# Kernel tuning notes

Measured on AMD Instinct MI355X. Metric: run time of the kernel, lower is better.

## Reference

```python
import jax, jax.numpy as jnp
import numpy as np

K_HOPS = 3  # spektral TAGConv default
BN_EPS = 1e-3  # keras BatchNormalization default epsilon


def _propagate(x, edge_src, edge_dst, edge_weight, n_nodes):
    # y[dst] += w * x[src]  (sparse adjacency @ x)
    msg = x[edge_src] * edge_weight[:, None]
    return jax.ops.segment_sum(msg, edge_dst, num_segments=n_nodes)


def _tag_conv(x, edge_src, edge_dst, edge_weight, W, b):
    n = x.shape[0]
    hops = [x]
    h = x
    for _ in range(K_HOPS):
        h = _propagate(h, edge_src, edge_dst, edge_weight, n)
        hops.append(h)
    # concat hops along features then dense combine: [N, F*(K+1)] @ [F*(K+1), C]
    return jnp.concatenate(hops, axis=-1) @ W + b


def setup_inputs() -> dict:
    key = jax.random.key(0)
    ks = jax.random.split(key, 6)
    N, F, E, H, L = 20000, 2000, 640000, 128, 15
    x = jax.random.normal(ks[0], (N, F), dtype=jnp.float32)
    edge_src = jax.random.randint(ks[1], (E,), 0, N, dtype=jnp.int32)
    edge_dst = jax.random.randint(ks[2], (E,), 0, N, dtype=jnp.int32)
    # normalized adjacency weights, roughly 1/avg_degree scale
    edge_weight = jax.random.uniform(ks[3], (E,), dtype=jnp.float32) / 32.0
    W1 = jax.random.normal(ks[4], (F * (K_HOPS + 1), H), dtype=jnp.float32) * (1.0 / np.sqrt(F * (K_HOPS + 1)))
    b1 = jnp.zeros((H,), dtype=jnp.float32)
    gamma = jnp.ones((H,), dtype=jnp.float32)
    beta = jnp.zeros((H,), dtype=jnp.float32)
    moving_mean = jnp.zeros((H,), dtype=jnp.float32)
    moving_var = jnp.ones((H,), dtype=jnp.float32)
    W2 = jax.random.normal(ks[5], (H * (K_HOPS + 1), L), dtype=jnp.float32) * (1.0 / np.sqrt(H * (K_HOPS + 1)))
    b2 = jnp.zeros((L,), dtype=jnp.float32)
    return {"x": x, "edge_src": edge_src, "edge_dst": edge_dst, "edge_weight": edge_weight,
            "W1": W1, "b1": b1, "gamma": gamma, "beta": beta,
            "moving_mean": moving_mean, "moving_var": moving_var, "W2": W2, "b2": b2}


def reference(x, edge_src, edge_dst, edge_weight, W1, b1, gamma, beta,
              moving_mean, moving_var, W2, b2):
    # training=False: Dropout is identity, BN uses moving statistics
    h = _tag_conv(x, edge_src, edge_dst, edge_weight, W1, b1)
    h = (h - moving_mean) * jax.lax.rsqrt(moving_var + BN_EPS) * gamma + beta
    h = jax.nn.relu(h)
    z = _tag_conv(h, edge_src, edge_dst, edge_weight, W2, b2)
    return z
```

## Files before the change

kernel.cpp:

```cpp
#include <hip/hip_runtime.h>
#include <cstdint>
#include <cstddef>

#define N_NODES 20000
#define F_IN    2000
#define H_DIM   128
#define L_DIM   15
#define K_PAD   2048
#define M_PAD   20096
#define N1      512
#define BM      128
#define BN      128
#define BK      32

typedef __attribute__((ext_vector_type(4))) float f32x4;
typedef __attribute__((ext_vector_type(8))) short s16x8;
typedef __attribute__((ext_vector_type(8))) unsigned short u16x8;

__device__ __forceinline__ unsigned short f2bf(float f) {
  unsigned int u = __float_as_uint(f);
  u += 0x7fff + ((u >> 16) & 1);
  return (unsigned short)(u >> 16);
}

__global__ __launch_bounds__(256) void k_cvt_x(const float* __restrict__ x,
                                               unsigned short* __restrict__ xb) {
  unsigned int t = blockIdx.x * 256u + threadIdx.x;
  unsigned int row = t >> 8;
  unsigned int colB = (t & 255u) * 8u;
  u16x8 o = {0, 0, 0, 0, 0, 0, 0, 0};
  if (row < N_NODES && colB < F_IN) {
    const float4 a = *(const float4*)(x + (size_t)row * F_IN + colB);
    const float4 b = *(const float4*)(x + (size_t)row * F_IN + colB + 4);
    o[0] = f2bf(a.x); o[1] = f2bf(a.y); o[2] = f2bf(a.z); o[3] = f2bf(a.w);
    o[4] = f2bf(b.x); o[5] = f2bf(b.y); o[6] = f2bf(b.z); o[7] = f2bf(b.w);
  }
  *(u16x8*)(xb + (size_t)t * 8) = o;
}

__global__ __launch_bounds__(256) void k_cvt_w1(const float* __restrict__ W1,
                                                unsigned short* __restrict__ bt) {
  __shared__ unsigned short tile[128 * 67];
  const int hop = blockIdx.x >> 5;
  const int k0  = (blockIdx.x & 31) * 64;
  const int t = threadIdx.x;
#pragma unroll
  for (int it = 0; it < 8; ++it) {
    int f4 = it * 256 + t;
    int r  = f4 >> 5;
    int c4 = f4 & 31;
    int k = k0 + r;
    float4 v = make_float4(0.f, 0.f, 0.f, 0.f);
    if (k < F_IN) v = *(const float4*)(W1 + (size_t)(hop * F_IN + k) * H_DIM + c4 * 4);
    tile[(c4 * 4 + 0) * 67 + r] = f2bf(v.x);
    tile[(c4 * 4 + 1) * 67 + r] = f2bf(v.y);
    tile[(c4 * 4 + 2) * 67 + r] = f2bf(v.z);
    tile[(c4 * 4 + 3) * 67 + r] = f2bf(v.w);
  }
  __syncthreads();
  const int c = t >> 1, kh = (t & 1) * 32;
  unsigned short* dst = bt + (size_t)(hop * 128 + c) * K_PAD + k0 + kh;
  const unsigned short* srcp = tile + c * 67 + kh;
#pragma unroll
  for (int q = 0; q < 4; ++q) {
    u16x8 o;
#pragma unroll
    for (int e = 0; e < 8; ++e) o[e] = srcp[q * 8 + e];
    *(u16x8*)(dst + q * 8) = o;
  }
}

__global__ __launch_bounds__(256) void k_gemm1(const unsigned short* __restrict__ A,
                                               const unsigned short* __restrict__ B,
                                               float* __restrict__ C) {
  __shared__ unsigned short As[BM * BK];
  __shared__ unsigned short Bs[BN * BK];
  const int b = blockIdx.x;
  const int i_tile = (b & 7) + 8 * (b >> 5);
  const int j_tile = (b >> 3) & 3;
  if (i_tile >= M_PAD / BM) return;
  const int rowA0 = i_tile * BM;
  const int colB0 = j_tile * BN;
  const int tid  = threadIdx.x;
  const int lane = tid & 63;
  const int wave = tid >> 6;
  const int wm = (wave >> 1) * 64;
  const int wn = (wave & 1) * 64;
  const int quad = lane >> 4;
  const int l15  = lane & 15;
  f32x4 acc[4][4] = {};

  for (int kt = 0; kt < K_PAD; kt += BK) {
#pragma unroll
    for (int r = 0; r < 2; ++r) {
      int c = r * 256 + tid;
      int row = c >> 2;
      int kc = (c & 3) * 8;
      const unsigned short* ga = A + (size_t)(rowA0 + row) * K_PAD + kt + kc;
      __builtin_amdgcn_global_load_lds((const __attribute__((address_space(1))) void*)ga,
                                       (__attribute__((address_space(3))) void*)(As + c * 8),
                                       16, 0, 0);
      const unsigned short* gb = B + (size_t)(colB0 + row) * K_PAD + kt + kc;
      __builtin_amdgcn_global_load_lds((const __attribute__((address_space(1))) void*)gb,
                                       (__attribute__((address_space(3))) void*)(Bs + c * 8),
                                       16, 0, 0);
    }
    __syncthreads();
    s16x8 af[4], bfr[4];
#pragma unroll
    for (int i = 0; i < 4; ++i)
      af[i] = *(const s16x8*)(As + (wm + i * 16 + l15) * BK + quad * 8);
#pragma unroll
    for (int j = 0; j < 4; ++j)
      bfr[j] = *(const s16x8*)(Bs + (wn + j * 16 + l15) * BK + quad * 8);
#pragma unroll
    for (int i = 0; i < 4; ++i)
#pragma unroll
      for (int j = 0; j < 4; ++j)
        acc[i][j] = __builtin_amdgcn_mfma_f32_16x16x32_bf16(af[i], bfr[j], acc[i][j], 0, 0, 0);
    __syncthreads();
  }

#pragma unroll
  for (int i = 0; i < 4; ++i) {
    int row0 = rowA0 + wm + i * 16 + quad * 4;
#pragma unroll
    for (int j = 0; j < 4; ++j) {
      int col = colB0 + wn + j * 16 + l15;
#pragma unroll
      for (int r = 0; r < 4; ++r) {
        int row = row0 + r;
        if (row < N_NODES) C[(size_t)row * N1 + col] = acc[i][j][r];
      }
    }
  }
}

__global__ __launch_bounds__(256) void k_hist(const int* __restrict__ dst,
                                              int* __restrict__ deg, int E) {
  int i = blockIdx.x * 256 + threadIdx.x;
  int e = i * 4;
  if (e + 4 <= E) {
    int4 d4 = *(const int4*)(dst + e);
    atomicAdd(&deg[d4.x], 1); atomicAdd(&deg[d4.y], 1);
    atomicAdd(&deg[d4.z], 1); atomicAdd(&deg[d4.w], 1);
  } else {
    for (; e < E; ++e) atomicAdd(&deg[dst[e]], 1);
  }
}

__global__ __launch_bounds__(1024) void k_scan(const int* __restrict__ deg,
                                               int* __restrict__ rowStart,
                                               int* __restrict__ cursor) {
  __shared__ int sums[1024];
  const int t = threadIdx.x;
  const int chunk = (N_NODES + 1023) / 1024;
  int lo = t * chunk;
  int hi = lo + chunk; if (hi > N_NODES) hi = N_NODES;
  int s = 0;
  for (int i = lo; i < hi; ++i) s += deg[i];
  sums[t] = s;
  __syncthreads();
  for (int off = 1; off < 1024; off <<= 1) {
    int v = sums[t];
    int u = (t >= off) ? sums[t - off] : 0;
    __syncthreads();
    sums[t] = v + u;
    __syncthreads();
  }
  int run = sums[t] - s;
  for (int i = lo; i < hi; ++i) {
    rowStart[i] = run; cursor[i] = run; run += deg[i];
  }
  if (t == 1023) rowStart[N_NODES] = run;
}

__global__ __launch_bounds__(256) void k_scatter(const int* __restrict__ src,
                                                 const int* __restrict__ dst,
                                                 const float* __restrict__ w,
                                                 int* cursor,
                                                 int2* __restrict__ eSW, int E) {
  int e = blockIdx.x * 256 + threadIdx.x;
  if (e >= E) return;
  int p = atomicAdd(&cursor[dst[e]], 1);
  eSW[p] = make_int2(src[e], __float_as_int(w[e]));
}

__global__ __launch_bounds__(256) void k_prop128(const int* __restrict__ rowStart,
    const int2* __restrict__ eSW,
    const float* __restrict__ in, int inStride, int inOff,
    const float* __restrict__ addv, int addStride, int addOff,
    float* __restrict__ out,
    const float* __restrict__ b1, const float* __restrict__ gamma,
    const float* __restrict__ beta, const float* __restrict__ mean,
    const float* __restrict__ var, int doBN) {
  const int lane = threadIdx.x & 63;
  const int d = blockIdx.x * 4 + (threadIdx.x >> 6);
  const int s0 = rowStart[d], s1 = rowStart[d + 1];
  const int c2 = lane * 2;
  float2 acc = make_float2(0.f, 0.f);
  int j = s0;
  for (; j + 8 <= s1; j += 8) {
    int2 e0 = eSW[j],     e1 = eSW[j + 1], e2 = eSW[j + 2], e3 = eSW[j + 3];
    int2 e4 = eSW[j + 4], e5 = eSW[j + 5], e6 = eSW[j + 6], e7 = eSW[j + 7];
    float2 v0 = *(const float2*)(in + (size_t)e0.x * inStride + inOff + c2);
    float2 v1 = *(const float2*)(in + (size_t)e1.x * inStride + inOff + c2);
    float2 v2 = *(const float2*)(in + (size_t)e2.x * inStride + inOff + c2);
    float2 v3 = *(const float2*)(in + (size_t)e3.x * inStride + inOff + c2);
    float2 v4 = *(const float2*)(in + (size_t)e4.x * inStride + inOff + c2);
    float2 v5 = *(const float2*)(in + (size_t)e5.x * inStride + inOff + c2);
    float2 v6 = *(const float2*)(in + (size_t)e6.x * inStride + inOff + c2);
    float2 v7 = *(const float2*)(in + (size_t)e7.x * inStride + inOff + c2);
    float w0 = __int_as_float(e0.y), w1 = __int_as_float(e1.y);
    float w2 = __int_as_float(e2.y), w3 = __int_as_float(e3.y);
    float w4 = __int_as_float(e4.y), w5 = __int_as_float(e5.y);
    float w6 = __int_as_float(e6.y), w7 = __int_as_float(e7.y);
    acc.x = fmaf(w0, v0.x, acc.x); acc.y = fmaf(w0, v0.y, acc.y);
    acc.x = fmaf(w1, v1.x, acc.x); acc.y = fmaf(w1, v1.y, acc.y);
    acc.x = fmaf(w2, v2.x, acc.x); acc.y = fmaf(w2, v2.y, acc.y);
    acc.x = fmaf(w3, v3.x, acc.x); acc.y = fmaf(w3, v3.y, acc.y);
    acc.x = fmaf(w4, v4.x, acc.x); acc.y = fmaf(w4, v4.y, acc.y);
    acc.x = fmaf(w5, v5.x, acc.x); acc.y = fmaf(w5, v5.y, acc.y);
    acc.x = fmaf(w6, v6.x, acc.x); acc.y = fmaf(w6, v6.y, acc.y);
    acc.x = fmaf(w7, v7.x, acc.x); acc.y = fmaf(w7, v7.y, acc.y);
  }
  for (; j + 4 <= s1; j += 4) {
    int2 e0 = eSW[j], e1 = eSW[j + 1], e2 = eSW[j + 2], e3 = eSW[j + 3];
    float2 v0 = *(const float2*)(in + (size_t)e0.x * inStride + inOff + c2);
    float2 v1 = *(const float2*)(in + (size_t)e1.x * inStride + inOff + c2);
    float2 v2 = *(const float2*)(in + (size_t)e2.x * inStride + inOff + c2);
    float2 v3 = *(const float2*)(in + (size_t)e3.x * inStride + inOff + c2);
    float w0 = __int_as_float(e0.y), w1 = __int_as_float(e1.y);
    float w2 = __int_as_float(e2.y), w3 = __int_as_float(e3.y);
    acc.x = fmaf(w0, v0.x, acc.x); acc.y = fmaf(w0, v0.y, acc.y);
    acc.x = fmaf(w1, v1.x, acc.x); acc.y = fmaf(w1, v1.y, acc.y);
    acc.x = fmaf(w2, v2.x, acc.x); acc.y = fmaf(w2, v2.y, acc.y);
    acc.x = fmaf(w3, v3.x, acc.x); acc.y = fmaf(w3, v3.y, acc.y);
  }
  for (; j < s1; ++j) {
    int2 e = eSW[j];
    float2 v = *(const float2*)(in + (size_t)e.x * inStride + inOff + c2);
    float w = __int_as_float(e.y);
    acc.x = fmaf(w, v.x, acc.x); acc.y = fmaf(w, v.y, acc.y);
  }
  float2 av = *(const float2*)(addv + (size_t)d * addStride + addOff + c2);
  float r0 = av.x + acc.x, r1 = av.y + acc.y;
  if (doBN) {
    float2 bb = *(const float2*)(b1 + c2);
    float2 gg = *(const float2*)(gamma + c2);
    float2 be = *(const float2*)(beta + c2);
    float2 mm = *(const float2*)(mean + c2);
    float2 vv = *(const float2*)(var + c2);
    r0 = (r0 + bb.x - mm.x) * rsqrtf(vv.x + 1e-3f) * gg.x + be.x;
    r1 = (r1 + bb.y - mm.y) * rsqrtf(vv.y + 1e-3f) * gg.y + be.y;
    r0 = r0 > 0.f ? r0 : 0.f;
    r1 = r1 > 0.f ? r1 : 0.f;
  }
  *(float2*)(out + (size_t)d * H_DIM + c2) = make_float2(r0, r1);
}

__global__ __launch_bounds__(256) void k_gemm2(const float* __restrict__ Hh,
                                               const float* __restrict__ W2,
                                               float* __restrict__ Y2) {
  __shared__ float w2s[512 * 15];
  for (int i = threadIdx.x; i < 512 * 15; i += 256) w2s[i] = W2[i];
  __syncthreads();
  const int c = threadIdx.x & 63;
  const int d = blockIdx.x * 4 + (threadIdx.x >> 6);
  if (c >= 60 || d >= N_NODES) return;
  const int hop = c / 15, j = c % 15;
  const float4* hr4 = (const float4*)(Hh + (size_t)d * H_DIM);
  float acc = 0.f;
#pragma unroll 8
  for (int k4 = 0; k4 < 32; ++k4) {
    float4 h = hr4[k4];
    const float* wp = w2s + ((hop << 7) + k4 * 4) * 15 + j;
    acc = fmaf(h.x, wp[0],  acc);
    acc = fmaf(h.y, wp[15], acc);
    acc = fmaf(h.z, wp[30], acc);
    acc = fmaf(h.w, wp[45], acc);
  }
  Y2[(size_t)d * 60 + c] = acc;
}

__global__ __launch_bounds__(256) void k_prop15(const int* __restrict__ rowStart,
    const int2* __restrict__ eSW,
    const float* __restrict__ in, int inStride, int inOff,
    const float* __restrict__ addv, int addStride, int addOff,
    const float* __restrict__ bias, float* __restrict__ out) {
  const int f = threadIdx.x & 15;
  const int d = blockIdx.x * 16 + (threadIdx.x >> 4);
  if (f >= 15) return;
  const int s0 = rowStart[d], s1 = rowStart[d + 1];
  float acc = 0.f;
  int j = s0;
  for (; j + 4 <= s1; j += 4) {
    int2 e0 = eSW[j], e1 = eSW[j + 1], e2 = eSW[j + 2], e3 = eSW[j + 3];
    float v0 = in[(size_t)e0.x * inStride + inOff + f];
    float v1 = in[(size_t)e1.x * inStride + inOff + f];
    float v2 = in[(size_t)e2.x * inStride + inOff + f];
    float v3 = in[(size_t)e3.x * inStride + inOff + f];
    acc = fmaf(__int_as_float(e0.y), v0, acc);
    acc = fmaf(__int_as_float(e1.y), v1, acc);
    acc = fmaf(__int_as_float(e2.y), v2, acc);
    acc = fmaf(__int_as_float(e3.y), v3, acc);
  }
  for (; j < s1; ++j) {
    int2 e = eSW[j];
    acc = fmaf(__int_as_float(e.y), in[(size_t)e.x * inStride + inOff + f], acc);
  }
  float b = bias ? bias[f] : 0.f;
  out[(size_t)d * 15 + f] = addv[(size_t)d * addStride + addOff + f] + acc + b;
}

extern "C" void kernel_launch(void* const* d_in, const int* in_sizes, int n_in,
                              void* d_out, int out_size, void* d_ws, size_t ws_size,
                              hipStream_t stream) {
  const float* x     = (const float*)d_in[0];
  const int*   esrc  = (const int*)d_in[1];
  const int*   edst  = (const int*)d_in[2];
  const float* ew    = (const float*)d_in[3];
  const float* W1    = (const float*)d_in[4];
  const float* b1    = (const float*)d_in[5];
  const float* gamma = (const float*)d_in[6];
  const float* beta  = (const float*)d_in[7];
  const float* mmean = (const float*)d_in[8];
  const float* mvar  = (const float*)d_in[9];
  const float* W2    = (const float*)d_in[10];
  const float* b2    = (const float*)d_in[11];
  const int E = in_sizes[1];
  char* ws = (char*)d_ws;

  unsigned short* xb  = (unsigned short*)(ws);
  unsigned short* w1r = (unsigned short*)(ws + 82313216);
  float* Y        = (float*)(ws + 84410368);
  int*   deg      = (int*)(ws + 125370368);
  int*   rowStart = (int*)(ws + 125450496);
  int*   cursor   = (int*)(ws + 125530624);
  int2*  eSW      = (int2*)(ws + 125610752);
  float* P   = (float*)(ws);
  float* Q   = (float*)(ws + 10240000);
  float* Hb  = (float*)(ws + 20480000);
  float* Y2  = (float*)(ws + 30720000);
  float* zP  = (float*)(ws + 35520000);
  float* zQ  = (float*)(ws + 36720000);
  float* zout = (float*)d_out;

  hipMemsetAsync(deg, 0, N_NODES * sizeof(int), stream);
  k_hist<<<(E / 4 + 255) / 256 + 1, 256, 0, stream>>>(edst, deg, E);
  k_scan<<<1, 1024, 0, stream>>>(deg, rowStart, cursor);
  k_scatter<<<(E + 255) / 256, 256, 0, stream>>>(esrc, edst, ew, cursor, eSW, E);

  k_cvt_x<<<(M_PAD * K_PAD / 8) / 256, 256, 0, stream>>>(x, xb);
  k_cvt_w1<<<128, 256, 0, stream>>>(W1, w1r);
  k_gemm1<<<640, 256, 0, stream>>>(xb, w1r, Y);

  k_prop128<<<N_NODES / 4, 256, 0, stream>>>(rowStart, eSW, Y, N1, 3 * H_DIM, Y, N1, 2 * H_DIM, P,
                                             b1, gamma, beta, mmean, mvar, 0);
  k_prop128<<<N_NODES / 4, 256, 0, stream>>>(rowStart, eSW, P, H_DIM, 0, Y, N1, 1 * H_DIM, Q,
                                             b1, gamma, beta, mmean, mvar, 0);
  k_prop128<<<N_NODES / 4, 256, 0, stream>>>(rowStart, eSW, Q, H_DIM, 0, Y, N1, 0, Hb,
                                             b1, gamma, beta, mmean, mvar, 1);

  k_gemm2<<<N_NODES / 4, 256, 0, stream>>>(Hb, W2, Y2);
  k_prop15<<<N_NODES / 16, 256, 0, stream>>>(rowStart, eSW, Y2, 60, 45, Y2, 60, 30, nullptr, zP);
  k_prop15<<<N_NODES / 16, 256, 0, stream>>>(rowStart, eSW, zP, 15, 0, Y2, 60, 15, nullptr, zQ);
  k_prop15<<<N_NODES / 16, 256, 0, stream>>>(rowStart, eSW, zQ, 15, 0, Y2, 60, 0, b2, zout);
}
```

Measured before the change: 633.6 us.

## Fuse x bf16 conversion into GEMM1, split-K, and gather bf16 in propagation

Drops the separate x-to-bf16 conversion pass by converting fp32 x inside the GEMM1 A-tile load. GEMM1 now splits K into two halves, which doubles the block count for more parallelism, and a new combine kernel sums the two partial outputs. The propagation kernels now gather bf16 intermediate features instead of fp32, halving gather traffic. In exchange, A tiles are loaded synchronously through registers rather than by direct global-to-LDS loads, the combine adds an extra pass, and the bf16 intermediates lose some precision.

After: 641.4 us. Within noise of the previous version (+1.2%).

```diff
diff --git a/kernel.cpp b/kernel.cpp
--- a/kernel.cpp
+++ b/kernel.cpp
@@ -1,4 +1,5 @@
 #include <hip/hip_runtime.h>
+#include <hip/hip_bf16.h>
 #include <cstdint>
 #include <cstddef>
 
@@ -7,15 +8,16 @@
 #define H_DIM   128
 #define L_DIM   15
 #define K_PAD   2048
-#define M_PAD   20096
 #define N1      512
 #define BM      128
 #define BN      128
 #define BK      32
+#define I_TILES 157
 
 typedef __attribute__((ext_vector_type(4))) float f32x4;
 typedef __attribute__((ext_vector_type(8))) short s16x8;
 typedef __attribute__((ext_vector_type(8))) unsigned short u16x8;
+typedef __attribute__((ext_vector_type(4))) unsigned int u32x4;
 
 __device__ __forceinline__ unsigned short f2bf(float f) {
   unsigned int u = __float_as_uint(f);
@@ -23,19 +25,17 @@
   return (unsigned short)(u >> 16);
 }
 
-__global__ __launch_bounds__(256) void k_cvt_x(const float* __restrict__ x,
-                                               unsigned short* __restrict__ xb) {
-  unsigned int t = blockIdx.x * 256u + threadIdx.x;
-  unsigned int row = t >> 8;
-  unsigned int colB = (t & 255u) * 8u;
-  u16x8 o = {0, 0, 0, 0, 0, 0, 0, 0};
-  if (row < N_NODES && colB < F_IN) {
-    const float4 a = *(const float4*)(x + (size_t)row * F_IN + colB);
-    const float4 b = *(const float4*)(x + (size_t)row * F_IN + colB + 4);
-    o[0] = f2bf(a.x); o[1] = f2bf(a.y); o[2] = f2bf(a.z); o[3] = f2bf(a.w);
-    o[4] = f2bf(b.x); o[5] = f2bf(b.y); o[6] = f2bf(b.z); o[7] = f2bf(b.w);
-  }
-  *(u16x8*)(xb + (size_t)t * 8) = o;
+__device__ __forceinline__ unsigned int pkbf(float a, float b) {
+  union { __hip_bfloat162 h; unsigned int u; } cv;
+  cv.h = __float22bfloat162_rn(make_float2(a, b));
+  return cv.u;
+}
+
+__device__ __forceinline__ float2 bf2f(unsigned int u) {
+  float2 r;
+  r.x = __uint_as_float(u << 16);
+  r.y = __uint_as_float(u & 0xffff0000u);
+  return r;
 }
 
 __global__ __launch_bounds__(256) void k_cvt_w1(const float* __restrict__ W1,
@@ -70,15 +70,18 @@
   }
 }
 
-__global__ __launch_bounds__(256) void k_gemm1(const unsigned short* __restrict__ A,
+__global__ __launch_bounds__(256) void k_gemm1(const float* __restrict__ X,
                                                const unsigned short* __restrict__ B,
-                                               float* __restrict__ C) {
+                                               float* __restrict__ C0,
+                                               float* __restrict__ C1) {
   __shared__ unsigned short As[BM * BK];
   __shared__ unsigned short Bs[BN * BK];
   const int b = blockIdx.x;
-  const int i_tile = (b & 7) + 8 * (b >> 5);
-  const int j_tile = (b >> 3) & 3;
-  if (i_tile >= M_PAD / BM) return;
+  const int i_tile = (b & 7) + 8 * (b >> 6);
+  const int mid = (b >> 3) & 7;
+  const int j_tile = mid & 3;
+  const int ks = mid >> 2;
+  if (i_tile >= I_TILES) return;
   const int rowA0 = i_tile * BM;
   const int colB0 = j_tile * BN;
   const int tid  = threadIdx.x;
@@ -90,21 +93,37 @@
   const int l15  = lane & 15;
   f32x4 acc[4][4] = {};
 
-  for (int kt = 0; kt < K_PAD; kt += BK) {
+  const int kend = ks ? F_IN : 1024;
+  for (int kt = ks * 1024; kt < kend; kt += BK) {
 #pragma unroll
     for (int r = 0; r < 2; ++r) {
       int c = r * 256 + tid;
       int row = c >> 2;
       int kc = (c & 3) * 8;
-      const unsigned short* ga = A + (size_t)(rowA0 + row) * K_PAD + kt + kc;
-      __builtin_amdgcn_global_load_lds((const __attribute__((address_space(1))) void*)ga,
-                                       (__attribute__((address_space(3))) void*)(As + c * 8),
-                                       16, 0, 0);
       const unsigned short* gb = B + (size_t)(colB0 + row) * K_PAD + kt + kc;
       __builtin_amdgcn_global_load_lds((const __attribute__((address_space(1))) void*)gb,
                                        (__attribute__((address_space(3))) void*)(Bs + c * 8),
                                        16, 0, 0);
     }
+#pragma unroll
+    for (int r = 0; r < 2; ++r) {
+      int c = r * 256 + tid;
+      int row = c >> 2;
+      int kc = (c & 3) * 8;
+      int grow = rowA0 + row;
+      int gk = kt + kc;
+      float4 va = make_float4(0.f, 0.f, 0.f, 0.f);
+      float4 vb = make_float4(0.f, 0.f, 0.f, 0.f);
+      if (grow < N_NODES && gk < F_IN) {
+        const float* p = X + (size_t)grow * F_IN + gk;
+        va = *(const float4*)p;
+        vb = *(const float4*)(p + 4);
+      }
+      u32x4 w;
+      w.x = pkbf(va.x, va.y); w.y = pkbf(va.z, va.w);
+      w.z = pkbf(vb.x, vb.y); w.w = pkbf(vb.z, vb.w);
+      *(u32x4*)(As + (size_t)c * 8) = w;
+    }
     __syncthreads();
     s16x8 af[4], bfr[4];
 #pragma unroll
@@ -121,6 +140,7 @@
     __syncthreads();
   }
 
+  float* Cp = ks ? C1 : C0;
 #pragma unroll
   for (int i = 0; i < 4; ++i) {
     int row0 = rowA0 + wm + i * 16 + quad * 4;
@@ -130,9 +150,27 @@
 #pragma unroll
       for (int r = 0; r < 4; ++r) {
         int row = row0 + r;
-        if (row < N_NODES) C[(size_t)row * N1 + col] = acc[i][j][r];
+        if (row < N_NODES) Cp[(size_t)row * N1 + col] = acc[i][j][r];
       }
     }
+  }
+}
+
+__global__ __launch_bounds__(256) void k_comb(float* __restrict__ C0,
+                                              const float* __restrict__ C1,
+                                              unsigned short* __restrict__ Yb3) {
+  unsigned int t = blockIdx.x * 256u + threadIdx.x;
+  unsigned int row = t >> 7;
+  unsigned int c4 = (t & 127u) * 4u;
+  size_t idx = (size_t)row * N1 + c4;
+  float4 a = *(const float4*)(C0 + idx);
+  float4 b = *(const float4*)(C1 + idx);
+  float4 s = make_float4(a.x + b.x, a.y + b.y, a.z + b.z, a.w + b.w);
+  if (c4 < 384) {
+    *(float4*)(C0 + idx) = s;
+  } else {
+    unsigned int u0 = pkbf(s.x, s.y), u1 = pkbf(s.z, s.w);
+    *(uint2*)(Yb3 + (size_t)row * H_DIM + (c4 - 384)) = make_uint2(u0, u1);
   }
 }
 
@@ -186,11 +224,11 @@
   eSW[p] = make_int2(src[e], __float_as_int(w[e]));
 }
 
-__global__ __launch_bounds__(256) void k_prop128(const int* __restrict__ rowStart,
+__global__ __launch_bounds__(256) void k_prop128b(const int* __restrict__ rowStart,
     const int2* __restrict__ eSW,
-    const float* __restrict__ in, int inStride, int inOff,
+    const unsigned short* __restrict__ gsrc,
     const float* __restrict__ addv, int addStride, int addOff,
-    float* __restrict__ out,
+    unsigned short* __restrict__ outb, float* __restrict__ outf,
     const float* __restrict__ b1, const float* __restrict__ gamma,
     const float* __restrict__ beta, const float* __restrict__ mean,
     const float* __restrict__ var, int doBN) {
@@ -198,53 +236,42 @@
   const int d = blockIdx.x * 4 + (threadIdx.x >> 6);
   const int s0 = rowStart[d], s1 = rowStart[d + 1];
   const int c2 = lane * 2;
-  float2 acc = make_float2(0.f, 0.f);
+  float ax = 0.f, ay = 0.f;
   int j = s0;
   for (; j + 8 <= s1; j += 8) {
     int2 e0 = eSW[j],     e1 = eSW[j + 1], e2 = eSW[j + 2], e3 = eSW[j + 3];
     int2 e4 = eSW[j + 4], e5 = eSW[j + 5], e6 = eSW[j + 6], e7 = eSW[j + 7];
-    float2 v0 = *(const float2*)(in + (size_t)e0.x * inStride + inOff + c2);
-    float2 v1 = *(const float2*)(in + (size_t)e1.x * inStride + inOff + c2);
-    float2 v2 = *(const float2*)(in + (size_t)e2.x * inStride + inOff + c2);
-    float2 v3 = *(const float2*)(in + (size_t)e3.x * inStride + inOff + c2);
-    float2 v4 = *(const float2*)(in + (size_t)e4.x * inStride + inOff + c2);
-    float2 v5 = *(const float2*)(in + (size_t)e5.x * inStride + inOff + c2);
-    float2 v6 = *(const float2*)(in + (size_t)e6.x * inStride + inOff + c2);
-    float2 v7 = *(const float2*)(in + (size_t)e7.x * inStride + inOff + c2);
+    unsigned int g0 = *(const unsigned int*)(gsrc + (size_t)e0.x * H_DIM + c2);
+    unsigned int g1 = *(const unsigned int*)(gsrc + (size_t)e1.x * H_DIM + c2);
+    unsigned int g2 = *(const unsigned int*)(gsrc + (size_t)e2.x * H_DIM + c2);
+    unsigned int g3 = *(const unsigned int*)(gsrc + (size_t)e3.x * H_DIM + c2);
+    unsigned int g4 = *(const unsigned int*)(gsrc + (size_t)e4.x * H_DIM + c2);
+    unsigned int g5 = *(const unsigned int*)(gsrc + (size_t)e5.x * H_DIM + c2);
+    unsigned int g6 = *(const unsigned int*)(gsrc + (size_t)e6.x * H_DIM + c2);
+    unsigned int g7 = *(const unsigned int*)(gsrc + (size_t)e7.x * H_DIM + c2);
+    float2 v0 = bf2f(g0), v1 = bf2f(g1), v2 = bf2f(g2), v3 = bf2f(g3);
+    float2 v4 = bf2f(g4), v5 = bf2f(g5), v6 = bf2f(g6), v7 = bf2f(g7);
     float w0 = __int_as_float(e0.y), w1 = __int_as_float(e1.y);
     float w2 = __int_as_float(e2.y), w3 = __int_as_float(e3.y);
     float w4 = __int_as_float(e4.y), w5 = __int_as_float(e5.y);
     float w6 = __int_as_float(e6.y), w7 = __int_as_float(e7.y);
-    acc.x = fmaf(w0, v0.x, acc.x); acc.y = fmaf(w0, v0.y, acc.y);
-    acc.x = fmaf(w1, v1.x, acc.x); acc.y = fmaf(w1, v1.y, acc.y);
-    acc.x = fmaf(w2, v2.x, acc.x); acc.y = fmaf(w2, v2.y, acc.y);
-    acc.x = fmaf(w3, v3.x, acc.x); acc.y = fmaf(w3, v3.y, acc.y);
-    acc.x = fmaf(w4, v4.x, acc.x); acc.y = fmaf(w4, v4.y, acc.y);
-    acc.x = fmaf(w5, v5.x, acc.x); acc.y = fmaf(w5, v5.y, acc.y);
-    acc.x = fmaf(w6, v6.x, acc.x); acc.y = fmaf(w6, v6.y, acc.y);
-    acc.x = fmaf(w7, v7.x, acc.x); acc.y = fmaf(w7, v7.y, acc.y);
-  }
-  for (; j + 4 <= s1; j += 4) {
-    int2 e0 = eSW[j], e1 = eSW[j + 1], e2 = eSW[j + 2], e3 = eSW[j + 3];
-    float2 v0 = *(const float2*)(in + (size_t)e0.x * inStride + inOff + c2);
-    float2 v1 = *(const float2*)(in + (size_t)e1.x * inStride + inOff + c2);
-    float2 v2 = *(const float2*)(in + (size_t)e2.x * inStride + inOff + c2);
-    float2 v3 = *(const float2*)(in + (size_t)e3.x * inStride + inOff + c2);
-    float w0 = __int_as_float(e0.y), w1 = __int_as_float(e1.y);
-    float w2 = __int_as_float(e2.y), w3 = __int_as_float(e3.y);
-    acc.x = fmaf(w0, v0.x, acc.x); acc.y = fmaf(w0, v0.y, acc.y);
-    acc.x = fmaf(w1, v1.x, acc.x); acc.y = fmaf(w1, v1.y, acc.y);
-    acc.x = fmaf(w2, v2.x, acc.x); acc.y = fmaf(w2, v2.y, acc.y);
-    acc.x = fmaf(w3, v3.x, acc.x); acc.y = fmaf(w3, v3.y, acc.y);
+    ax = fmaf(w0, v0.x, ax); ay = fmaf(w0, v0.y, ay);
+    ax = fmaf(w1, v1.x, ax); ay = fmaf(w1, v1.y, ay);
+    ax = fmaf(w2, v2.x, ax); ay = fmaf(w2, v2.y, ay);
+    ax = fmaf(w3, v3.x, ax); ay = fmaf(w3, v3.y, ay);
+    ax = fmaf(w4, v4.x, ax); ay = fmaf(w4, v4.y, ay);
+    ax = fmaf(w5, v5.x, ax); ay = fmaf(w5, v5.y, ay);
+    ax = fmaf(w6, v6.x, ax); ay = fmaf(w6, v6.y, ay);
+    ax = fmaf(w7, v7.x, ax); ay = fmaf(w7, v7.y, ay);
   }
   for (; j < s1; ++j) {
     int2 e = eSW[j];
-    float2 v = *(const float2*)(in + (size_t)e.x * inStride + inOff + c2);
+    float2 v = bf2f(*(const unsigned int*)(gsrc + (size_t)e.x * H_DIM + c2));
     float w = __int_as_float(e.y);
-    acc.x = fmaf(w, v.x, acc.x); acc.y = fmaf(w, v.y, acc.y);
+    ax = fmaf(w, v.x, ax); ay = fmaf(w, v.y, ay);
   }
   float2 av = *(const float2*)(addv + (size_t)d * addStride + addOff + c2);
-  float r0 = av.x + acc.x, r1 = av.y + acc.y;
+  float r0 = av.x + ax, r1 = av.y + ay;
   if (doBN) {
     float2 bb = *(const float2*)(b1 + c2);
     float2 gg = *(const float2*)(gamma + c2);
@@ -255,8 +282,10 @@
     r1 = (r1 + bb.y - mm.y) * rsqrtf(vv.y + 1e-3f) * gg.y + be.y;
     r0 = r0 > 0.f ? r0 : 0.f;
     r1 = r1 > 0.f ? r1 : 0.f;
-  }
-  *(float2*)(out + (size_t)d * H_DIM + c2) = make_float2(r0, r1);
+    *(float2*)(outf + (size_t)d * H_DIM + c2) = make_float2(r0, r1);
+  } else {
+    *(unsigned int*)(outb + (size_t)d * H_DIM + c2) = pkbf(r0, r1);
+  }
 }
 
 __global__ __launch_bounds__(256) void k_gemm2(const float* __restrict__ Hh,
@@ -331,36 +360,38 @@
   const int E = in_sizes[1];
   char* ws = (char*)d_ws;
 
-  unsigned short* xb  = (unsigned short*)(ws);
-  unsigned short* w1r = (unsigned short*)(ws + 82313216);
-  float* Y        = (float*)(ws + 84410368);
-  int*   deg      = (int*)(ws + 125370368);
-  int*   rowStart = (int*)(ws + 125450496);
-  int*   cursor   = (int*)(ws + 125530624);
-  int2*  eSW      = (int2*)(ws + 125610752);
-  float* P   = (float*)(ws);
-  float* Q   = (float*)(ws + 10240000);
-  float* Hb  = (float*)(ws + 20480000);
-  float* Y2  = (float*)(ws + 30720000);
-  float* zP  = (float*)(ws + 35520000);
-  float* zQ  = (float*)(ws + 36720000);
-  float* zout = (float*)d_out;
+  float*          C0   = (float*)(ws);
+  float*          C1   = (float*)(ws + 40960000);
+  unsigned short* Yb3  = (unsigned short*)(ws + 81920000);
+  unsigned short* w1r  = (unsigned short*)(ws + 87040000);
+  int2*           eSW  = (int2*)(ws + 89137152);
+  int*            deg      = (int*)(ws + 94257152);
+  int*            rowStart = (int*)(ws + 94337280);
+  int*            cursor   = (int*)(ws + 94417408);
+  unsigned short* P   = (unsigned short*)(ws + 40960000);
+  unsigned short* Q   = (unsigned short*)(ws + 46080000);
+  float*          Hb  = (float*)(ws + 51200000);
+  float*          Y2  = (float*)(ws + 61440000);
+  float*          zP  = (float*)(ws + 66240000);
+  float*          zQ  = (float*)(ws + 67440000);
+  float*          Y   = C0;
+  float*          zout = (float*)d_out;
 
   hipMemsetAsync(deg, 0, N_NODES * sizeof(int), stream);
   k_hist<<<(E / 4 + 255) / 256 + 1, 256, 0, stream>>>(edst, deg, E);
   k_scan<<<1, 1024, 0, stream>>>(deg, rowStart, cursor);
   k_scatter<<<(E + 255) / 256, 256, 0, stream>>>(esrc, edst, ew, cursor, eSW, E);
 
-  k_cvt_x<<<(M_PAD * K_PAD / 8) / 256, 256, 0, stream>>>(x, xb);
   k_cvt_w1<<<128, 256, 0, stream>>>(W1, w1r);
-  k_gemm1<<<640, 256, 0, stream>>>(xb, w1r, Y);
-
-  k_prop128<<<N_NODES / 4, 256, 0, stream>>>(rowStart, eSW, Y, N1, 3 * H_DIM, Y, N1, 2 * H_DIM, P,
-                                             b1, gamma, beta, mmean, mvar, 0);
-  k_prop128<<<N_NODES / 4, 256, 0, stream>>>(rowStart, eSW, P, H_DIM, 0, Y, N1, 1 * H_DIM, Q,
-                                             b1, gamma, beta, mmean, mvar, 0);
-  k_prop128<<<N_NODES / 4, 256, 0, stream>>>(rowStart, eSW, Q, H_DIM, 0, Y, N1, 0, Hb,
-                                             b1, gamma, beta, mmean, mvar, 1);
+  k_gemm1<<<1280, 256, 0, stream>>>(x, w1r, C0, C1);
+  k_comb<<<(N_NODES * 128) / 256, 256, 0, stream>>>(C0, C1, Yb3);
+
+  k_prop128b<<<N_NODES / 4, 256, 0, stream>>>(rowStart, eSW, Yb3, Y, N1, 2 * H_DIM,
+                                              P, nullptr, b1, gamma, beta, mmean, mvar, 0);
+  k_prop128b<<<N_NODES / 4, 256, 0, stream>>>(rowStart, eSW, P, Y, N1, 1 * H_DIM,
+                                              Q, nullptr, b1, gamma, beta, mmean, mvar, 0);
+  k_prop128b<<<N_NODES / 4, 256, 0, stream>>>(rowStart, eSW, Q, Y, N1, 0,
+                                              nullptr, Hb, b1, gamma, beta, mmean, mvar, 1);
 
   k_gemm2<<<N_NODES / 4, 256, 0, stream>>>(Hb, W2, Y2);
   k_prop15<<<N_NODES / 16, 256, 0, stream>>>(rowStart, eSW, Y2, 60, 45, Y2, 60, 30, nullptr, zP);
```
